# Performance work log

Hardware: AMD Instinct MI355X
Metric: run time of the kernel (lower is better)

## Reference

```python
import jax, jax.numpy as jnp
import numpy as np

T = 2048
HIDDEN = 4096
NH = 32        # query heads
NKV = 8        # kv heads
G = NH // NKV  # GQA group size
D = 128        # head_dim (== v_head_dim)
ROPE_BASE = 1000000.0


def setup_inputs() -> dict:
    key = jax.random.key(0)
    ks = jax.random.split(key, 8)
    s = 0.02
    return {
        "positions": jnp.arange(T, dtype=jnp.int32),
        "hidden_states": jax.random.normal(ks[0], (T, HIDDEN), dtype=jnp.float32),
        "Wq": jax.random.normal(ks[1], (HIDDEN, NH * D), dtype=jnp.float32) * s,
        "bq": jnp.zeros((NH * D,), dtype=jnp.float32),
        "Wk": jax.random.normal(ks[2], (HIDDEN, NKV * D), dtype=jnp.float32) * s,
        "bk": jnp.zeros((NKV * D,), dtype=jnp.float32),
        "Wv": jax.random.normal(ks[3], (HIDDEN, NKV * D), dtype=jnp.float32) * s,
        "bv": jnp.zeros((NKV * D,), dtype=jnp.float32),
        "Wo": jax.random.normal(ks[4], (NH * D, HIDDEN), dtype=jnp.float32) * s,
    }


def _rope(positions, x):
    # neox-style rotary, full rotary_dim = D
    half = D // 2
    inv_freq = 1.0 / (ROPE_BASE ** (jnp.arange(0, half, dtype=jnp.float32) / half))
    freqs = positions.astype(jnp.float32)[:, None] * inv_freq[None, :]  # [T, half]
    cos = jnp.cos(freqs)[:, None, :]  # [T, 1, half]
    sin = jnp.sin(freqs)[:, None, :]
    x1, x2 = x[..., :half], x[..., half:]
    return jnp.concatenate([x1 * cos - x2 * sin, x2 * cos + x1 * sin], axis=-1)


def reference(positions, hidden_states, Wq, bq, Wk, bk, Wv, bv, Wo):
    q = (hidden_states @ Wq + bq).reshape(T, NH, D)
    k = (hidden_states @ Wk + bk).reshape(T, NKV, D)
    v = (hidden_states @ Wv + bv).reshape(T, NKV, D)
    q = _rope(positions, q)
    k = _rope(positions, k)

    scale = D ** -0.5
    qg = q.reshape(T, NKV, G, D)
    # scores: [NKV, G, T(query), S(key)]
    scores = jnp.einsum("tkgd,skd->kgts", qg, k) * scale
    causal = positions[:, None] >= positions[None, :]  # [T, S]
    scores = jnp.where(causal[None, None, :, :], scores, jnp.finfo(scores.dtype).min)
    probs = jax.nn.softmax(scores, axis=-1)
    attn = jnp.einsum("kgts,skd->tkgd", probs, v).reshape(T, NH * D)

    output = attn @ Wo
    kv_fused = jnp.stack([k, v], axis=0)  # [2, T, NKV, D]
    return output, kv_fused
```

## Files before the change

kernel.cpp:

```cpp
#include <hip/hip_runtime.h>
#include <stdint.h>

#define T_SEQ 2048
#define HIDDEN_DIM 4096
#define NH 32
#define NKV 8
#define HD 128
#define QKV_N 6144

typedef unsigned short u16;
typedef __attribute__((__ext_vector_type__(8))) __bf16 bf16x8;
typedef __attribute__((__ext_vector_type__(4))) float f32x4;

__device__ __forceinline__ float exp2_fast(float x) {
    return __builtin_amdgcn_exp2f(x);
}

__device__ __forceinline__ u16 f2bf(float f) {
    union { float f; unsigned u; } x; x.f = f;
    unsigned u = x.u;
    unsigned r = u + 0x7FFFu + ((u >> 16) & 1u);
    return (u16)(r >> 16);
}
__device__ __forceinline__ float bf2f(u16 h) {
    union { unsigned u; float f; } x; x.u = ((unsigned)h) << 16;
    return x.f;
}

__device__ __forceinline__ void gl_lds16(const u16* g, u16* l) {
    __builtin_amdgcn_global_load_lds((__attribute__((address_space(1))) void*)g,
                                     (__attribute__((address_space(3))) void*)l,
                                     16, 0, 0);
}

#define BAR()                                  \
    {                                          \
        asm volatile("" ::: "memory");         \
        __builtin_amdgcn_s_barrier();          \
        asm volatile("" ::: "memory");         \
    }

template <int N>
__device__ __forceinline__ void vmwait() {
    if constexpr (N == 0) asm volatile("s_waitcnt vmcnt(0)" ::: "memory");
    else if constexpr (N == 3) asm volatile("s_waitcnt vmcnt(3)" ::: "memory");
    else if constexpr (N == 4) asm volatile("s_waitcnt vmcnt(4)" ::: "memory");
    else if constexpr (N == 6) asm volatile("s_waitcnt vmcnt(6)" ::: "memory");
    else if constexpr (N == 8) asm volatile("s_waitcnt vmcnt(8)" ::: "memory");
}

__global__ __launch_bounds__(256) void cast_f32_bf16(const float* __restrict__ in,
                                                     u16* __restrict__ out, int n4) {
    int i = blockIdx.x * 256 + threadIdx.x;
    if (i < n4) {
        float4 v = ((const float4*)in)[i];
        uint2 o;
        o.x = (unsigned)f2bf(v.x) | ((unsigned)f2bf(v.y) << 16);
        o.y = (unsigned)f2bf(v.z) | ((unsigned)f2bf(v.w) << 16);
        ((uint2*)out)[i] = o;
    }
}

__global__ __launch_bounds__(256) void transpose_cast(const float* __restrict__ W,
                                                      u16* __restrict__ Wt, int R, int C) {
    __shared__ float tile[64][65];
    const int tid = threadIdx.x;
    const int c0 = blockIdx.x * 64, r0 = blockIdx.y * 64;
    const int lr = tid >> 4;
    const int lc4 = tid & 15;
#pragma unroll
    for (int i = 0; i < 4; ++i) {
        float4 v = *(const float4*)&W[(size_t)(r0 + lr + 16 * i) * C + c0 + lc4 * 4];
        tile[lr + 16 * i][lc4 * 4 + 0] = v.x;
        tile[lr + 16 * i][lc4 * 4 + 1] = v.y;
        tile[lr + 16 * i][lc4 * 4 + 2] = v.z;
        tile[lr + 16 * i][lc4 * 4 + 3] = v.w;
    }
    __syncthreads();
    const int rr0 = (tid & 7) * 8;
    const int cc = tid >> 3;
#pragma unroll
    for (int i = 0; i < 2; ++i) {
        int c = cc + 32 * i;
        u16 tmp[8];
#pragma unroll
        for (int j = 0; j < 8; ++j) tmp[j] = f2bf(tile[rr0 + j][c]);
        *(uint4*)&Wt[(size_t)(c0 + c) * R + r0 + rr0] = *(const uint4*)tmp;
    }
}

__global__ __launch_bounds__(256) void concat_bias(const float* __restrict__ bq,
                                                   const float* __restrict__ bk,
                                                   const float* __restrict__ bv,
                                                   float* __restrict__ out) {
    int i = blockIdx.x * 256 + threadIdx.x;
    if (i < 4096) out[i] = bq[i];
    else if (i < 5120) out[i] = bk[i - 4096];
    else if (i < 6144) out[i] = bv[i - 5120];
}

#define KSTEP_2P(S, SLOT, STG, VMW)                                                          \
    {                                                                                        \
        bf16x8 bf_[3], af_[4];                                                               \
        _Pragma("unroll") for (int n = 0; n < 3; ++n)                                        \
            bf_[n] = *(const bf16x8*)&Bs[SLOT][boff[n]];                                     \
        _Pragma("unroll") for (int m = 0; m < 4; ++m)                                        \
            af_[m] = *(const bf16x8*)&As[SLOT][aoff[m]];                                     \
        if (STG) {                                                                           \
            gl_lds16(Ast + (size_t)((S) + 3) * 32, &As[((SLOT) + 3) & 3][ldsS0]);            \
            gl_lds16(Ast + (size_t)((S) + 3) * 32 + rowK128, &As[((SLOT) + 3) & 3][ldsS1]);  \
        }                                                                                    \
        BAR();                                                                               \
        __builtin_amdgcn_s_setprio(1);                                                       \
        _Pragma("unroll") for (int m = 0; m < 4; ++m)                                        \
            _Pragma("unroll") for (int n = 0; n < 3; ++n)                                    \
                acc[m][n] = __builtin_amdgcn_mfma_f32_16x16x32_bf16(af_[m], bf_[n],          \
                                                                    acc[m][n], 0, 0, 0);     \
        __builtin_amdgcn_s_setprio(0);                                                       \
        BAR();                                                                               \
        _Pragma("unroll") for (int m = 0; m < 4; ++m)                                        \
            af_[m] = *(const bf16x8*)&As[SLOT][aoff[4 + m]];                                 \
        if (STG) {                                                                           \
            gl_lds16(Bst + (size_t)((S) + 3) * 32, &Bs[((SLOT) + 3) & 3][ldsB0]);            \
            if (tid < 256)                                                                   \
                gl_lds16(BstH + (size_t)((S) + 3) * 32, &Bs[((SLOT) + 3) & 3][ldsB2]);       \
        }                                                                                    \
        BAR();                                                                               \
        __builtin_amdgcn_s_setprio(1);                                                       \
        _Pragma("unroll") for (int m = 0; m < 4; ++m)                                        \
            _Pragma("unroll") for (int n = 0; n < 3; ++n)                                    \
                acc[4 + m][n] = __builtin_amdgcn_mfma_f32_16x16x32_bf16(af_[m], bf_[n],      \
                                                                        acc[4 + m][n],       \
                                                                        0, 0, 0);            \
        __builtin_amdgcn_s_setprio(0);                                                       \
        asm volatile("s_waitcnt vmcnt(" #VMW ")" ::: "memory");                              \
        BAR();                                                                               \
    }

template <int BF16_OUT, int HAS_BIAS>
__global__ __launch_bounds__(512, 2) void gemm256(const u16* __restrict__ A,
                                                  const u16* __restrict__ Bt,
                                                  const float* __restrict__ bias,
                                                  void* __restrict__ Cv,
                                                  int M, int N, int K) {
    __shared__ alignas(16) u16 As[4][256 * 32];
    __shared__ alignas(16) u16 Bs[4][192 * 32];
    const int tid = threadIdx.x;
    const int wave = tid >> 6;
    const int lane = tid & 63;
    const int l15 = lane & 15;
    const int quad = lane >> 4;
    const int wr = wave >> 2;
    const int wc = wave & 3;

    const int nbn = N / 192;
    const int q8 = (int)gridDim.x >> 3;
    const int wg = blockIdx.x;
    const int swz = (wg & 7) * q8 + (wg >> 3);
    const int m0 = (swz / nbn) * 256;
    const int n0 = (swz % nbn) * 192;

    const int srow = tid >> 2;
    const int schunk = (tid & 3) ^ ((tid >> 3) & 3);
    const u16* Ast = A + (size_t)(m0 + srow) * K + schunk * 8;
    const u16* Bst = Bt + (size_t)(n0 + srow) * K + schunk * 8;
    const u16* BstH = Bt + (size_t)(n0 + 128 + srow) * K + schunk * 8;
    const size_t rowK128 = (size_t)128 * K;
    const int ldsS0 = wave * 512;
    const int ldsS1 = 4096 + wave * 512;
    const int ldsB0 = wave * 512;
    const int ldsB2 = 4096 + wave * 512;

    int aoff[8], boff[3];
#pragma unroll
    for (int m = 0; m < 8; ++m) {
        int row = wr * 128 + m * 16 + l15;
        aoff[m] = row * 32 + ((quad ^ ((row >> 1) & 3)) << 3);
    }
#pragma unroll
    for (int n = 0; n < 3; ++n) {
        int row = wc * 48 + n * 16 + l15;
        boff[n] = row * 32 + ((quad ^ ((row >> 1) & 3)) << 3);
    }

    f32x4 acc[8][3] = {};
    const int NS = K >> 5;

#pragma unroll
    for (int s = 0; s < 3; ++s) {
        gl_lds16(Ast + (size_t)s * 32, &As[s][ldsS0]);
        gl_lds16(Ast + (size_t)s * 32 + rowK128, &As[s][ldsS1]);
        gl_lds16(Bst + (size_t)s * 32, &Bs[s][ldsB0]);
        if (tid < 256) gl_lds16(BstH + (size_t)s * 32, &Bs[s][ldsB2]);
    }
    asm volatile("s_waitcnt vmcnt(6)" ::: "memory");
    BAR();

#pragma unroll 1
    for (int s = 0; s < NS - 4; s += 4) {
        KSTEP_2P(s, 0, 1, 6)
        KSTEP_2P(s + 1, 1, 1, 6)
        KSTEP_2P(s + 2, 2, 1, 6)
        KSTEP_2P(s + 3, 3, 1, 6)
    }
    {
        const int s = NS - 4;
        KSTEP_2P(s, 0, 1, 6)
        KSTEP_2P(s + 1, 1, 0, 6)
        KSTEP_2P(s + 2, 2, 0, 0)
        KSTEP_2P(s + 3, 3, 0, 0)
    }

#pragma unroll
    for (int m = 0; m < 8; ++m) {
        const int row = m0 + wr * 128 + m * 16 + quad * 4;
#pragma unroll
        for (int n = 0; n < 3; ++n) {
            const int col = n0 + wc * 48 + n * 16 + l15;
            float b = HAS_BIAS ? bias[col] : 0.f;
#pragma unroll
            for (int r = 0; r < 4; ++r) {
                float v = acc[m][n][r] + b;
                if (BF16_OUT) ((u16*)Cv)[(size_t)(row + r) * N + col] = f2bf(v);
                else ((float*)Cv)[(size_t)(row + r) * N + col] = v;
            }
        }
    }
}

#define STAGE(SL, S)                                                                         \
    {                                                                                        \
        const size_t ko_ = (size_t)(S) * 32;                                                 \
        _Pragma("unroll") for (int c_ = 0; c_ < ACALLS; ++c_)                                \
            gl_lds16(Ast + ko_ + (size_t)(c_ * 128) * K, &As[SL][c_ * 4096 + wave * 512]);   \
        _Pragma("unroll") for (int c_ = 0; c_ < BFULL; ++c_)                                 \
            gl_lds16(Bst + ko_ + (size_t)(c_ * 128) * K, &Bs[SL][c_ * 4096 + wave * 512]);   \
        if (BHALF) gl_lds16(BstH + ko_, &Bs[SL][BFULL * 4096 + (wave & 3) * 512]);           \
    }

#define REGION(SLOT, NSLOT, CA, CB, NA, NB, RN)                                              \
    {                                                                                        \
        if (RN) {                                                                            \
            _Pragma("unroll") for (int n_ = 0; n_ < NF; ++n_)                                \
                NB[n_] = *(const bf16x8*)&Bs[NSLOT][boff[n_]];                               \
            _Pragma("unroll") for (int m_ = 0; m_ < MF; ++m_)                                \
                NA[m_] = *(const bf16x8*)&As[NSLOT][aoff[m_]];                               \
        }                                                                                    \
        __builtin_amdgcn_s_setprio(1);                                                       \
        _Pragma("unroll") for (int m_ = 0; m_ < MF; ++m_)                                    \
            _Pragma("unroll") for (int n_ = 0; n_ < NF; ++n_)                                \
                acc[m_][n_] = __builtin_amdgcn_mfma_f32_16x16x32_bf16(CA[m_], CB[n_],        \
                                                                      acc[m_][n_], 0, 0, 0); \
        __builtin_amdgcn_s_setprio(0);                                                       \
    }

#define KSTEP_RA(S, SLOT, STG, VMW, RN, CA, CB, NA, NB)       \
    {                                                         \
        if (STG) STAGE((((SLOT) + 3) & 3), (S) + 3)           \
        vmwait<VMW>();                                        \
        BAR();                                                \
        REGION(SLOT, (((SLOT) + 1) & 3), CA, CB, NA, NB, RN)  \
        BAR();                                                \
    }

template <int MF, int NF, int ACALLS, int BFULL, int BHALF, int BF16_OUT, int HAS_BIAS>
__global__ __launch_bounds__(512, 2) void gemm_ph(const u16* __restrict__ A,
                                                  const u16* __restrict__ Bt,
                                                  const float* __restrict__ bias,
                                                  void* __restrict__ Cv,
                                                  int M, int N, int K) {
    constexpr int BM = MF * 32;
    constexpr int BN = NF * 64;
    constexpr int LPS = ACALLS + BFULL + BHALF;
    __shared__ alignas(16) u16 As[4][BM * 32];
    __shared__ alignas(16) u16 Bs[4][BN * 32];
    const int tid = threadIdx.x;
    const int wave = tid >> 6;
    const int lane = tid & 63;
    const int l15 = lane & 15;
    const int quad = lane >> 4;
    const int wr = wave >> 2;
    const int wc = wave & 3;

    const int nbn = N / BN;
    const int q8 = (int)gridDim.x >> 3;
    const int wg = blockIdx.x;
    const int swz = (wg & 7) * q8 + (wg >> 3);
    const int m0 = (swz / nbn) * BM;
    const int n0 = (swz % nbn) * BN;

    const int srow = tid >> 2;
    const int schunk = (tid & 3) ^ ((tid >> 3) & 3);
    const u16* Ast = A + (size_t)(m0 + srow) * K + schunk * 8;
    const u16* Bst = Bt + (size_t)(n0 + srow) * K + schunk * 8;
    const int srowH = (tid & 255) >> 2;
    const u16* BstH = Bt + (size_t)(n0 + BFULL * 128 + srowH) * K + schunk * 8;

    int aoff[MF], boff[NF];
#pragma unroll
    for (int m = 0; m < MF; ++m) {
        int row = wr * (MF * 16) + m * 16 + l15;
        aoff[m] = row * 32 + ((quad ^ ((row >> 1) & 3)) << 3);
    }
#pragma unroll
    for (int n = 0; n < NF; ++n) {
        int row = wc * (NF * 16) + n * 16 + l15;
        boff[n] = row * 32 + ((quad ^ ((row >> 1) & 3)) << 3);
    }

    bf16x8 fA0[MF], fB0[NF], fA1[MF], fB1[NF];
    f32x4 acc[MF][NF] = {};
    const int NS = K >> 5;

    STAGE(0, 0) STAGE(1, 1) STAGE(2, 2)
    vmwait<LPS>();
    BAR();
#pragma unroll
    for (int n = 0; n < NF; ++n) fB0[n] = *(const bf16x8*)&Bs[0][boff[n]];
#pragma unroll
    for (int m = 0; m < MF; ++m) fA0[m] = *(const bf16x8*)&As[0][aoff[m]];

#pragma unroll 1
    for (int s = 0; s < NS - 4; s += 4) {
        KSTEP_RA(s, 0, 1, 2 * LPS, 1, fA0, fB0, fA1, fB1)
        KSTEP_RA(s + 1, 1, 1, 2 * LPS, 1, fA1, fB1, fA0, fB0)
        KSTEP_RA(s + 2, 2, 1, 2 * LPS, 1, fA0, fB0, fA1, fB1)
        KSTEP_RA(s + 3, 3, 1, 2 * LPS, 1, fA1, fB1, fA0, fB0)
    }
    {
        const int s = NS - 4;
        KSTEP_RA(s, 0, 1, 2 * LPS, 1, fA0, fB0, fA1, fB1)
        KSTEP_RA(s + 1, 1, 0, LPS, 1, fA1, fB1, fA0, fB0)
        KSTEP_RA(s + 2, 2, 0, 0, 1, fA0, fB0, fA1, fB1)
        KSTEP_RA(s + 3, 3, 0, 0, 0, fA1, fB1, fA0, fB0)
    }

#pragma unroll
    for (int m = 0; m < MF; ++m) {
        const int row = m0 + wr * (MF * 16) + m * 16 + quad * 4;
#pragma unroll
        for (int n = 0; n < NF; ++n) {
            const int col = n0 + wc * (NF * 16) + n * 16 + l15;
            float b = HAS_BIAS ? bias[col] : 0.f;
#pragma unroll
            for (int r = 0; r < 4; ++r) {
                float v = acc[m][n][r] + b;
                if (BF16_OUT) ((u16*)Cv)[(size_t)(row + r) * N + col] = f2bf(v);
                else ((float*)Cv)[(size_t)(row + r) * N + col] = v;
            }
        }
    }
}

__global__ __launch_bounds__(256) void rope_kernel(const int* __restrict__ positions,
                                                   const u16* __restrict__ qkv,
                                                   u16* __restrict__ qh,
                                                   u16* __restrict__ kh,
                                                   u16* __restrict__ vt,
                                                   float* __restrict__ kv_out) {
    const int t = blockIdx.x;
    const float pos = (float)positions[t];
    const size_t rowbase = (size_t)t * QKV_N;
    const float nlog = -13.815510557964274f / 64.f;
    const float KZ = 0.08838834764831845f * 1.4426950408889634f;
    for (int col = threadIdx.x; col < QKV_N; col += 256) {
        if (col < 4096) {
            int hh = col >> 7, d = col & 127, j = d & 63;
            float ang = pos * __expf((float)j * nlog);
            float cs = cosf(ang), sn = sinf(ang);
            size_t base = rowbase + (size_t)(col & ~127);
            float x1 = bf2f(qkv[base + j]);
            float x2 = bf2f(qkv[base + 64 + j]);
            float v = (d < 64) ? (x1 * cs - x2 * sn) : (x2 * cs + x1 * sn);
            qh[((size_t)hh * T_SEQ + t) * HD + d] = f2bf(v * KZ);
        } else if (col < 5120) {
            int lc = col - 4096, hh = lc >> 7, d = lc & 127, j = d & 63;
            float ang = pos * __expf((float)j * nlog);
            float cs = cosf(ang), sn = sinf(ang);
            size_t base = rowbase + 4096 + (size_t)hh * 128;
            float x1 = bf2f(qkv[base + j]);
            float x2 = bf2f(qkv[base + 64 + j]);
            float v = (d < 64) ? (x1 * cs - x2 * sn) : (x2 * cs + x1 * sn);
            kh[((size_t)hh * T_SEQ + t) * HD + d] = f2bf(v);
            kv_out[((size_t)t * NKV + hh) * HD + d] = v;
        } else {
            int lc = col - 5120, hh = lc >> 7, d = lc & 127;
            float v = bf2f(qkv[rowbase + 5120 + (size_t)hh * 128 + d]);
            vt[((size_t)hh * HD + d) * T_SEQ + t] = f2bf(v);
            kv_out[(((size_t)T_SEQ + t) * NKV + hh) * HD + d] = v;
        }
    }
}

#define KS_STRIDE 136
#define VS_STRIDE 72
#define PS_STRIDE 72

__global__ __launch_bounds__(256) void attn_kernel(const u16* __restrict__ Qh,
                                                   const u16* __restrict__ Kh,
                                                   const u16* __restrict__ Vt,
                                                   u16* __restrict__ attn_out) {
    __shared__ alignas(16) u16 Ks[64 * KS_STRIDE];
    __shared__ alignas(16) u16 Vs[128 * VS_STRIDE];
    __shared__ alignas(16) u16 Ps[4][32 * PS_STRIDE];

    const int h = blockIdx.y;
    const int x = blockIdx.x;
    const int zig = (x & 1) ? ((x - 1) >> 1) : (15 - (x >> 1));
    const int qb = (h < 16) ? zig : (15 - zig);
    const int tid = threadIdx.x;
    const int wave = tid >> 6;
    const int lane = tid & 63;
    const int l15 = lane & 15;
    const int quad = lane >> 4;
    const int kvh = h >> 2;
    const int wrow0 = qb * 128 + wave * 32;

    const u16* Qp = Qh + ((size_t)h * T_SEQ + wrow0) * HD;
    const u16* Kp = Kh + (size_t)kvh * T_SEQ * HD;
    const u16* Vp = Vt + (size_t)kvh * HD * T_SEQ;

    bf16x8 aQ[2][4];
#pragma unroll
    for (int i = 0; i < 2; ++i)
#pragma unroll
        for (int kb = 0; kb < 4; ++kb)
            aQ[i][kb] = *(const bf16x8*)&Qp[(size_t)(i * 16 + l15) * HD + kb * 32 + quad * 8];

    bf16x8 ones;
#pragma unroll
    for (int z = 0; z < 8; ++z) ones[z] = (__bf16)1.0f;

    f32x4 acc[2][8] = {};
    f32x4 accl[2] = {};

    const int n_tiles = 2 * qb + 2;

    const int krow = tid >> 4;
    const int kcol = (tid & 15) * 8;
    const int vrow = tid >> 3;
    const int vcol = (tid & 7) * 8;

#pragma unroll 1
    for (int t = 0; t < n_tiles; ++t) {
        const int s0 = t * 64;
        __syncthreads();
#pragma unroll
        for (int rep = 0; rep < 4; ++rep) {
            int r = krow + rep * 16;
            *(uint4*)&Ks[r * KS_STRIDE + kcol] =
                *(const uint4*)&Kp[(size_t)(s0 + r) * HD + kcol];
        }
#pragma unroll
        for (int rep = 0; rep < 4; ++rep) {
            int d = vrow + rep * 32;
            *(uint4*)&Vs[d * VS_STRIDE + vcol] =
                *(const uint4*)&Vp[(size_t)d * T_SEQ + s0 + vcol];
        }
        __syncthreads();

        if (s0 <= wrow0 + 31) {
            f32x4 sc[2][4];
#pragma unroll
            for (int j = 0; j < 4; ++j) {
                f32x4 sa = {}, sb = {};
#pragma unroll
                for (int kb = 0; kb < 4; ++kb) {
                    bf16x8 bK = *(const bf16x8*)&Ks[(j * 16 + l15) * KS_STRIDE + kb * 32 + quad * 8];
                    sa = __builtin_amdgcn_mfma_f32_16x16x32_bf16(aQ[0][kb], bK, sa, 0, 0, 0);
                    sb = __builtin_amdgcn_mfma_f32_16x16x32_bf16(aQ[1][kb], bK, sb, 0, 0, 0);
                }
                sc[0][j] = sa;
                sc[1][j] = sb;
            }
#pragma unroll
            for (int i = 0; i < 2; ++i)
#pragma unroll
                for (int r = 0; r < 4; ++r) {
                    int t_idx = wrow0 + i * 16 + quad * 4 + r;
#pragma unroll
                    for (int j = 0; j < 4; ++j) {
                        int s_idx = s0 + j * 16 + l15;
                        float z = (s_idx > t_idx) ? -1e30f : sc[i][j][r];
                        float p = exp2_fast(z);
                        Ps[wave][(i * 16 + quad * 4 + r) * PS_STRIDE + j * 16 + l15] = f2bf(p);
                    }
                }
            bf16x8 aP[2][2];
#pragma unroll
            for (int i = 0; i < 2; ++i)
#pragma unroll
                for (int k2 = 0; k2 < 2; ++k2)
                    aP[i][k2] = *(const bf16x8*)&Ps[wave][(i * 16 + l15) * PS_STRIDE + k2 * 32 + quad * 8];
#pragma unroll
            for (int o = 0; o < 8; ++o) {
                bf16x8 bV0 = *(const bf16x8*)&Vs[(o * 16 + l15) * VS_STRIDE + quad * 8];
                bf16x8 bV1 = *(const bf16x8*)&Vs[(o * 16 + l15) * VS_STRIDE + 32 + quad * 8];
#pragma unroll
                for (int i = 0; i < 2; ++i) {
                    acc[i][o] = __builtin_amdgcn_mfma_f32_16x16x32_bf16(aP[i][0], bV0, acc[i][o], 0, 0, 0);
                    acc[i][o] = __builtin_amdgcn_mfma_f32_16x16x32_bf16(aP[i][1], bV1, acc[i][o], 0, 0, 0);
                }
            }
#pragma unroll
            for (int i = 0; i < 2; ++i) {
                accl[i] = __builtin_amdgcn_mfma_f32_16x16x32_bf16(aP[i][0], ones, accl[i], 0, 0, 0);
                accl[i] = __builtin_amdgcn_mfma_f32_16x16x32_bf16(aP[i][1], ones, accl[i], 0, 0, 0);
            }
        }
    }

#pragma unroll
    for (int i = 0; i < 2; ++i)
#pragma unroll
        for (int r = 0; r < 4; ++r) {
            float inv = 1.f / accl[i][r];
            int t_idx = wrow0 + i * 16 + quad * 4 + r;
#pragma unroll
            for (int o = 0; o < 8; ++o)
                attn_out[(size_t)t_idx * (NH * HD) + h * HD + o * 16 + l15] =
                    f2bf(acc[i][o][r] * inv);
        }
}

extern "C" void kernel_launch(void* const* d_in, const int* in_sizes, int n_in,
                              void* d_out, int out_size, void* d_ws, size_t ws_size,
                              hipStream_t stream) {
    const int* positions = (const int*)d_in[0];
    const float* hidden = (const float*)d_in[1];
    const float* Wq = (const float*)d_in[2];
    const float* bq = (const float*)d_in[3];
    const float* Wk = (const float*)d_in[4];
    const float* bk = (const float*)d_in[5];
    const float* Wv = (const float*)d_in[6];
    const float* bv = (const float*)d_in[7];
    const float* Wo = (const float*)d_in[8];

    char* ws = (char*)d_ws;
    u16* hs_bf   = (u16*)(ws + 0);
    u16* attnbuf = (u16*)(ws + 0);
    u16* wqkvT   = (u16*)(ws + 16777216);
    u16* woT     = (u16*)(ws + 16777216);
    u16* qkvbuf  = (u16*)(ws + 67108864);
    u16* qbuf    = (u16*)(ws + 92274688);
    u16* kbuf    = (u16*)(ws + 109051904);
    u16* vtbuf   = (u16*)(ws + 113246208);
    float* biasb = (float*)(ws + 117440512);

    float* out0 = (float*)d_out;
    float* kvout = out0 + (size_t)T_SEQ * HIDDEN_DIM;

    cast_f32_bf16<<<dim3((T_SEQ * HIDDEN_DIM / 4 + 255) / 256), dim3(256), 0, stream>>>(
        hidden, hs_bf, T_SEQ * HIDDEN_DIM / 4);
    transpose_cast<<<dim3(64, 64), dim3(256), 0, stream>>>(Wq, wqkvT, HIDDEN_DIM, 4096);
    transpose_cast<<<dim3(16, 64), dim3(256), 0, stream>>>(Wk, wqkvT + (size_t)4096 * HIDDEN_DIM, HIDDEN_DIM, 1024);
    transpose_cast<<<dim3(16, 64), dim3(256), 0, stream>>>(Wv, wqkvT + (size_t)5120 * HIDDEN_DIM, HIDDEN_DIM, 1024);
    concat_bias<<<dim3(24), dim3(256), 0, stream>>>(bq, bk, bv, biasb);

    gemm256<1, 1><<<dim3((T_SEQ / 256) * (QKV_N / 192)), dim3(512), 0, stream>>>(
        hs_bf, wqkvT, biasb, qkvbuf, T_SEQ, QKV_N, HIDDEN_DIM);

    transpose_cast<<<dim3(64, 64), dim3(256), 0, stream>>>(Wo, woT, NH * HD, HIDDEN_DIM);

    rope_kernel<<<dim3(T_SEQ), dim3(256), 0, stream>>>(positions, qkvbuf, qbuf, kbuf, vtbuf, kvout);

    attn_kernel<<<dim3(16, NH), dim3(256), 0, stream>>>(qbuf, kbuf, vtbuf, attnbuf);

    gemm_ph<4, 4, 1, 2, 0, 0, 0><<<dim3((T_SEQ / 128) * (HIDDEN_DIM / 256)), dim3(512), 0, stream>>>(
        attnbuf, woT, nullptr, out0, T_SEQ, HIDDEN_DIM, NH * HD);
}
```

Baseline: 528.1 us.

## Shrink QKV GEMM tile to 128x192 and simplify k-step pipeline

Replaces the 256x192 QKV projection GEMM tile with a 128x192 tile. This doubles the grid to 512 workgroups and raises the occupancy hint to 4. The two-phase k-step, with its interleaved partial A loads and mid-step barriers, becomes a single phase: issue prefetch, wait on vmcnt, barrier, then 12 MFMAs per wave. Each workgroup now has 2 workgroups' worth of work per CU to hide memory latency and reduce tail imbalance. The cost is lower arithmetic intensity per tile, meaning more global and LDS traffic for B, and less overlap of LDS reads with MFMA inside each step.

```diff
diff --git a/kernel.cpp b/kernel.cpp
--- a/kernel.cpp
+++ b/kernel.cpp
@@ -99,51 +99,40 @@
     else if (i < 6144) out[i] = bv[i - 5120];
 }
 
-#define KSTEP_2P(S, SLOT, STG, VMW)                                                          \
-    {                                                                                        \
-        bf16x8 bf_[3], af_[4];                                                               \
-        _Pragma("unroll") for (int n = 0; n < 3; ++n)                                        \
-            bf_[n] = *(const bf16x8*)&Bs[SLOT][boff[n]];                                     \
-        _Pragma("unroll") for (int m = 0; m < 4; ++m)                                        \
-            af_[m] = *(const bf16x8*)&As[SLOT][aoff[m]];                                     \
-        if (STG) {                                                                           \
-            gl_lds16(Ast + (size_t)((S) + 3) * 32, &As[((SLOT) + 3) & 3][ldsS0]);            \
-            gl_lds16(Ast + (size_t)((S) + 3) * 32 + rowK128, &As[((SLOT) + 3) & 3][ldsS1]);  \
-        }                                                                                    \
-        BAR();                                                                               \
-        __builtin_amdgcn_s_setprio(1);                                                       \
-        _Pragma("unroll") for (int m = 0; m < 4; ++m)                                        \
-            _Pragma("unroll") for (int n = 0; n < 3; ++n)                                    \
-                acc[m][n] = __builtin_amdgcn_mfma_f32_16x16x32_bf16(af_[m], bf_[n],          \
-                                                                    acc[m][n], 0, 0, 0);     \
-        __builtin_amdgcn_s_setprio(0);                                                       \
-        BAR();                                                                               \
-        _Pragma("unroll") for (int m = 0; m < 4; ++m)                                        \
-            af_[m] = *(const bf16x8*)&As[SLOT][aoff[4 + m]];                                 \
-        if (STG) {                                                                           \
-            gl_lds16(Bst + (size_t)((S) + 3) * 32, &Bs[((SLOT) + 3) & 3][ldsB0]);            \
-            if (tid < 256)                                                                   \
-                gl_lds16(BstH + (size_t)((S) + 3) * 32, &Bs[((SLOT) + 3) & 3][ldsB2]);       \
-        }                                                                                    \
-        BAR();                                                                               \
-        __builtin_amdgcn_s_setprio(1);                                                       \
-        _Pragma("unroll") for (int m = 0; m < 4; ++m)                                        \
-            _Pragma("unroll") for (int n = 0; n < 3; ++n)                                    \
-                acc[4 + m][n] = __builtin_amdgcn_mfma_f32_16x16x32_bf16(af_[m], bf_[n],      \
-                                                                        acc[4 + m][n],       \
-                                                                        0, 0, 0);            \
-        __builtin_amdgcn_s_setprio(0);                                                       \
-        asm volatile("s_waitcnt vmcnt(" #VMW ")" ::: "memory");                              \
-        BAR();                                                                               \
+#define KSTEP_128(S, SLOT, STG, VMW)                                                       \
+    {                                                                                      \
+        if (STG) {                                                                         \
+            const size_t ko_ = (size_t)((S) + 3) * 32;                                     \
+            gl_lds16(Ast + ko_, &As[((SLOT) + 3) & 3][wave * 512]);                        \
+            gl_lds16(Bst + ko_, &Bs[((SLOT) + 3) & 3][wave * 512]);                        \
+            gl_lds16(BstH + ko_, &Bs[((SLOT) + 3) & 3][4096 + (wave & 3) * 512]);          \
+        }                                                                                  \
+        vmwait<VMW>();                                                                     \
+        BAR();                                                                             \
+        {                                                                                  \
+            bf16x8 bf_[3], af_[4];                                                         \
+            _Pragma("unroll") for (int n = 0; n < 3; ++n)                                  \
+                bf_[n] = *(const bf16x8*)&Bs[SLOT][boff[n]];                               \
+            _Pragma("unroll") for (int m = 0; m < 4; ++m)                                  \
+                af_[m] = *(const bf16x8*)&As[SLOT][aoff[m]];                               \
+            __builtin_amdgcn_s_setprio(1);                                                 \
+            _Pragma("unroll") for (int m = 0; m < 4; ++m)                                  \
+                _Pragma("unroll") for (int n = 0; n < 3; ++n)                              \
+                    acc[m][n] = __builtin_amdgcn_mfma_f32_16x16x32_bf16(af_[m], bf_[n],    \
+                                                                        acc[m][n],         \
+                                                                        0, 0, 0);          \
+            __builtin_amdgcn_s_setprio(0);                                                 \
+        }                                                                                  \
+        BAR();                                                                             \
     }
 
 template <int BF16_OUT, int HAS_BIAS>
-__global__ __launch_bounds__(512, 2) void gemm256(const u16* __restrict__ A,
+__global__ __launch_bounds__(512, 4) void gemm128(const u16* __restrict__ A,
                                                   const u16* __restrict__ Bt,
                                                   const float* __restrict__ bias,
                                                   void* __restrict__ Cv,
                                                   int M, int N, int K) {
-    __shared__ alignas(16) u16 As[4][256 * 32];
+    __shared__ alignas(16) u16 As[4][128 * 32];
     __shared__ alignas(16) u16 Bs[4][192 * 32];
     const int tid = threadIdx.x;
     const int wave = tid >> 6;
@@ -157,24 +146,20 @@
     const int q8 = (int)gridDim.x >> 3;
     const int wg = blockIdx.x;
     const int swz = (wg & 7) * q8 + (wg >> 3);
-    const int m0 = (swz / nbn) * 256;
+    const int m0 = (swz / nbn) * 128;
     const int n0 = (swz % nbn) * 192;
 
     const int srow = tid >> 2;
     const int schunk = (tid & 3) ^ ((tid >> 3) & 3);
     const u16* Ast = A + (size_t)(m0 + srow) * K + schunk * 8;
     const u16* Bst = Bt + (size_t)(n0 + srow) * K + schunk * 8;
-    const u16* BstH = Bt + (size_t)(n0 + 128 + srow) * K + schunk * 8;
-    const size_t rowK128 = (size_t)128 * K;
-    const int ldsS0 = wave * 512;
-    const int ldsS1 = 4096 + wave * 512;
-    const int ldsB0 = wave * 512;
-    const int ldsB2 = 4096 + wave * 512;
-
-    int aoff[8], boff[3];
-#pragma unroll
-    for (int m = 0; m < 8; ++m) {
-        int row = wr * 128 + m * 16 + l15;
+    const int srowH = (tid & 255) >> 2;
+    const u16* BstH = Bt + (size_t)(n0 + 128 + srowH) * K + schunk * 8;
+
+    int aoff[4], boff[3];
+#pragma unroll
+    for (int m = 0; m < 4; ++m) {
+        int row = wr * 64 + m * 16 + l15;
         aoff[m] = row * 32 + ((quad ^ ((row >> 1) & 3)) << 3);
     }
 #pragma unroll
@@ -183,37 +168,36 @@
         boff[n] = row * 32 + ((quad ^ ((row >> 1) & 3)) << 3);
     }
 
-    f32x4 acc[8][3] = {};
+    f32x4 acc[4][3] = {};
     const int NS = K >> 5;
 
 #pragma unroll
     for (int s = 0; s < 3; ++s) {
-        gl_lds16(Ast + (size_t)s * 32, &As[s][ldsS0]);
-        gl_lds16(Ast + (size_t)s * 32 + rowK128, &As[s][ldsS1]);
-        gl_lds16(Bst + (size_t)s * 32, &Bs[s][ldsB0]);
-        if (tid < 256) gl_lds16(BstH + (size_t)s * 32, &Bs[s][ldsB2]);
-    }
-    asm volatile("s_waitcnt vmcnt(6)" ::: "memory");
+        gl_lds16(Ast + (size_t)s * 32, &As[s][wave * 512]);
+        gl_lds16(Bst + (size_t)s * 32, &Bs[s][wave * 512]);
+        gl_lds16(BstH + (size_t)s * 32, &Bs[s][4096 + (wave & 3) * 512]);
+    }
+    vmwait<6>();
     BAR();
 
 #pragma unroll 1
     for (int s = 0; s < NS - 4; s += 4) {
-        KSTEP_2P(s, 0, 1, 6)
-        KSTEP_2P(s + 1, 1, 1, 6)
-        KSTEP_2P(s + 2, 2, 1, 6)
-        KSTEP_2P(s + 3, 3, 1, 6)
+        KSTEP_128(s, 0, 1, 6)
+        KSTEP_128(s + 1, 1, 1, 6)
+        KSTEP_128(s + 2, 2, 1, 6)
+        KSTEP_128(s + 3, 3, 1, 6)
     }
     {
         const int s = NS - 4;
-        KSTEP_2P(s, 0, 1, 6)
-        KSTEP_2P(s + 1, 1, 0, 6)
-        KSTEP_2P(s + 2, 2, 0, 0)
-        KSTEP_2P(s + 3, 3, 0, 0)
-    }
-
-#pragma unroll
-    for (int m = 0; m < 8; ++m) {
-        const int row = m0 + wr * 128 + m * 16 + quad * 4;
+        KSTEP_128(s, 0, 1, 6)
+        KSTEP_128(s + 1, 1, 0, 3)
+        KSTEP_128(s + 2, 2, 0, 0)
+        KSTEP_128(s + 3, 3, 0, 0)
+    }
+
+#pragma unroll
+    for (int m = 0; m < 4; ++m) {
+        const int row = m0 + wr * 64 + m * 16 + quad * 4;
 #pragma unroll
         for (int n = 0; n < 3; ++n) {
             const int col = n0 + wc * 48 + n * 16 + l15;
@@ -557,7 +541,7 @@
     transpose_cast<<<dim3(16, 64), dim3(256), 0, stream>>>(Wv, wqkvT + (size_t)5120 * HIDDEN_DIM, HIDDEN_DIM, 1024);
     concat_bias<<<dim3(24), dim3(256), 0, stream>>>(bq, bk, bv, biasb);
 
-    gemm256<1, 1><<<dim3((T_SEQ / 256) * (QKV_N / 192)), dim3(512), 0, stream>>>(
+    gemm128<1, 1><<<dim3((T_SEQ / 128) * (QKV_N / 192)), dim3(512), 0, stream>>>(
         hs_bf, wqkvT, biasb, qkvbuf, T_SEQ, QKV_N, HIDDEN_DIM);
 
     transpose_cast<<<dim3(64, 64), dim3(256), 0, stream>>>(Wo, woT, NH * HD, HIDDEN_DIM);
```

New measurement: 550.6 us. 4.3% more time.
